# Performance work log

Measured on AMD Instinct MI355X. Metric: run time of the kernel, lower is better.

## Reference

```python
import jax, jax.numpy as jnp
import numpy as np


def setup_inputs() -> dict:
    key = jax.random.key(0)
    ks = jax.random.split(key, 6)
    B, S, D, E = 4, 8192, 2048, 8
    scale = 1.0 / np.sqrt(D)
    return {
        "x": jax.random.normal(ks[0], (B, S, D), dtype=jnp.float32),
        "Wg": jax.random.normal(ks[1], (E, D), dtype=jnp.float32) * scale,
        "bg": jax.random.normal(ks[2], (E,), dtype=jnp.float32) * scale,
        "Wn": jax.random.normal(ks[3], (E, D), dtype=jnp.float32) * scale,
        "bn": jax.random.normal(ks[4], (E,), dtype=jnp.float32) * scale,
        "noise": jax.random.normal(ks[5], (B, S, E), dtype=jnp.float32),
        "k": 2,
    }


def reference(x, Wg, bg, Wn, bn, noise, k):
    # gate and noisy-gate projections: [B,S,D] x [E,D] -> [B,S,E]
    gate_logits = jnp.einsum("bsd,ed->bse", x, Wg) + bg
    noisy_pre = jnp.einsum("bsd,ed->bse", x, Wn) + bn
    noisy_logits = noise * jax.nn.softplus(noisy_pre) + gate_logits

    # top-k over experts (largest, sorted), matching torch.topk
    topklogits, topexperts = jax.lax.top_k(noisy_logits, k)  # [B,S,k]

    # softmax over sparse logits (-inf elsewhere) == softmax over the topk
    # values, scattered back; small E,k so a one-hot scatter is cheap.
    topk_probs = jax.nn.softmax(topklogits, axis=-1)          # [B,S,k]
    onehot = jax.nn.one_hot(topexperts, noisy_logits.shape[-1],
                            dtype=topk_probs.dtype)           # [B,S,k,E]
    router_output = jnp.einsum("bsk,bske->bse", topk_probs, onehot)
    return router_output, topexperts
```

## Files before the change

kernel.cpp:

```cpp
#include <hip/hip_runtime.h>
#include <math.h>


#define RD 2048
#define RE 8
#define NE16 16
#define TOKB 64
#define CH 64
#define KSL 2
#define KLEN (RD / KSL)
#define NCH (KLEN / CH)
#define NW 4
#define REDW 20

#define AS1 __attribute__((address_space(1)))
#define AS3 __attribute__((address_space(3)))

__device__ __forceinline__ void gload_lds16(const float* g, float* l) {
    __builtin_amdgcn_global_load_lds((const AS1 unsigned int*)g,
                                     (AS3 unsigned int*)l, 16, 0, 0);
}

__global__ __launch_bounds__(256) void transpose_w_kernel(
    const float* __restrict__ Wg, const float* __restrict__ Wn,
    float* __restrict__ WT)
{
    const int idx = blockIdx.x * 256 + threadIdx.x;
    const int d = idx >> 4;
    const int e = idx & 15;
    WT[idx] = (e < 8) ? Wg[e * RD + d] : Wn[(e - 8) * RD + d];
}

__global__ __launch_bounds__(256) void router_main_kernel(
    const float* __restrict__ x,
    const float* __restrict__ WT,
    float* __restrict__ pws,
    int T)
{
    __shared__ float xb[2][TOKB * CH];

    const int tid = threadIdx.x;
    const int w = tid >> 6;
    const int l = tid & 63;
    const int kslice = blockIdx.x & 1;
    const int bt = blockIdx.x >> 1;
    const int tokBase = bt * TOKB;
    const int kbase = kslice * KLEN;

    float acc[NE16];
#pragma unroll
    for (int e = 0; e < NE16; ++e) acc[e] = 0.f;

    {
#pragma unroll
        for (int s = 0; s < 4; ++s) {
            const int t = (w * 4 + s) * 4 + (l >> 4);
            const int p = l & 15;
            const float* gsrc = x + (size_t)(tokBase + t) * RD + kbase
                                + ((p ^ (t & 7)) << 2);
            gload_lds16(gsrc, &xb[0][(w * 4 + s) * 256]);
        }
    }
    __syncthreads();

#pragma unroll 1
    for (int c = 0; c < NCH; ++c) {
        const int buf = c & 1;

        if (c + 1 < NCH) {
#pragma unroll
            for (int s = 0; s < 4; ++s) {
                const int t = (w * 4 + s) * 4 + (l >> 4);
                const int p = l & 15;
                const float* gsrc = x + (size_t)(tokBase + t) * RD + kbase
                                    + (c + 1) * CH + ((p ^ (t & 7)) << 2);
                gload_lds16(gsrc, &xb[buf ^ 1][(w * 4 + s) * 256]);
            }
        }

        const int wbase = __builtin_amdgcn_readfirstlane(
            (kbase + c * CH + w * 16) * NE16);
        const float* __restrict__ wt = WT + wbase;
#pragma unroll
        for (int r = 0; r < 4; ++r) {
            const int phys = (w * 4 + r) ^ (l & 7);
            const float4 xq = *reinterpret_cast<const float4*>(
                &xb[buf][l * CH + (phys << 2)]);
            const float xs[4] = {xq.x, xq.y, xq.z, xq.w};
#pragma unroll
            for (int ii = 0; ii < 4; ++ii) {
                const float* wrow = wt + (r * 4 + ii) * NE16;
#pragma unroll
                for (int e = 0; e < NE16; ++e)
                    acc[e] = fmaf(xs[ii], wrow[e], acc[e]);
            }
        }

        __syncthreads();
    }

    float* red = &xb[0][0];
    {
        const int roff = (w * TOKB + l) * REDW;
        *reinterpret_cast<float4*>(&red[roff + 0])  = make_float4(acc[0], acc[1], acc[2], acc[3]);
        *reinterpret_cast<float4*>(&red[roff + 4])  = make_float4(acc[4], acc[5], acc[6], acc[7]);
        *reinterpret_cast<float4*>(&red[roff + 8])  = make_float4(acc[8], acc[9], acc[10], acc[11]);
        *reinterpret_cast<float4*>(&red[roff + 12]) = make_float4(acc[12], acc[13], acc[14], acc[15]);
    }
    __syncthreads();

    {
        const int tok = tid >> 2;
        const int q = tid & 3;
        float4 s = make_float4(0.f, 0.f, 0.f, 0.f);
#pragma unroll
        for (int wv = 0; wv < NW; ++wv) {
            const float4 a = *reinterpret_cast<const float4*>(
                &red[(wv * TOKB + tok) * REDW + q * 4]);
            s.x += a.x; s.y += a.y; s.z += a.z; s.w += a.w;
        }
        float* dst = pws + ((size_t)kslice * T + tokBase + tok) * NE16 + q * 4;
        *reinterpret_cast<float4*>(dst) = s;
    }
}

__global__ __launch_bounds__(256) void router_finalize_kernel(
    const float* __restrict__ pws,
    const float* __restrict__ bg,
    const float* __restrict__ bn,
    const float* __restrict__ noise,
    float* __restrict__ out_router,
    float* __restrict__ out_experts,
    int T)
{
    const int tok = blockIdx.x * 256 + threadIdx.x;

    const float* p0 = pws + (size_t)tok * NE16;
    const float* p1 = pws + ((size_t)T + tok) * NE16;

    float g[RE], nn[RE];
#pragma unroll
    for (int e = 0; e < RE; ++e) {
        g[e]  = p0[e] + p1[e] + bg[e];
        nn[e] = p0[8 + e] + p1[8 + e] + bn[e];
    }

    const float4* nzp = reinterpret_cast<const float4*>(noise + (size_t)tok * RE);
    const float4 nz0 = nzp[0];
    const float4 nz1 = nzp[1];
    const float nzv[RE] = {nz0.x, nz0.y, nz0.z, nz0.w,
                           nz1.x, nz1.y, nz1.z, nz1.w};

    float v[RE];
#pragma unroll
    for (int e = 0; e < RE; ++e) {
        const float p = nn[e];
        const float sp = fmaxf(p, 0.f) + log1pf(expf(-fabsf(p)));
        v[e] = fmaf(nzv[e], sp, g[e]);
    }

    int i1 = 0; float m1 = v[0];
#pragma unroll
    for (int e = 1; e < RE; ++e)
        if (v[e] > m1) { m1 = v[e]; i1 = e; }
    int i2 = -1; float m2 = -INFINITY;
#pragma unroll
    for (int e = 0; e < RE; ++e)
        if (e != i1 && v[e] > m2) { m2 = v[e]; i2 = e; }

    const float e2 = expf(m2 - m1);
    const float inv = 1.f / (1.f + e2);
    const float p1s = inv;
    const float p2s = e2 * inv;

    float r[RE];
#pragma unroll
    for (int e = 0; e < RE; ++e)
        r[e] = (e == i1) ? p1s : ((e == i2) ? p2s : 0.f);

    float4* orow = reinterpret_cast<float4*>(out_router + (size_t)tok * RE);
    orow[0] = make_float4(r[0], r[1], r[2], r[3]);
    orow[1] = make_float4(r[4], r[5], r[6], r[7]);

    float2* erow = reinterpret_cast<float2*>(out_experts + (size_t)tok * 2);
    *erow = make_float2((float)i1, (float)i2);
}

extern "C" void kernel_launch(void* const* d_in, const int* in_sizes, int n_in,
                              void* d_out, int out_size, void* d_ws, size_t ws_size,
                              hipStream_t stream) {
    const float* x   = (const float*)d_in[0];
    const float* Wg  = (const float*)d_in[1];
    const float* bg  = (const float*)d_in[2];
    const float* Wn  = (const float*)d_in[3];
    const float* bn  = (const float*)d_in[4];
    const float* nz  = (const float*)d_in[5];
    const int T = in_sizes[0] / RD;

    float* WT  = (float*)d_ws;
    float* pws = WT + (size_t)RD * NE16;

    float* out_router  = (float*)d_out;
    float* out_experts = out_router + (size_t)T * RE;

    hipLaunchKernelGGL(transpose_w_kernel, dim3((RD * NE16) / 256), dim3(256),
                       0, stream, Wg, Wn, WT);

    const int blocks = (T / TOKB) * KSL;
    hipLaunchKernelGGL(router_main_kernel, dim3(blocks), dim3(256), 0,
                       stream, x, WT, pws, T);

    hipLaunchKernelGGL(router_finalize_kernel, dim3(T / 256), dim3(256), 0,
                       stream, pws, bg, bn, nz, out_router, out_experts, T);
}
```

Measured before the change: 62.23 us.

## Split K into four slices with smaller LDS chunks and kslice-major block order

Templates the main kernel on the number of K slices and launches four slices when the workspace allows, with a two-slice fallback otherwise. The LDS chunk shrinks from 64 to 32 columns, which halves shared memory per block and allows more resident blocks. Blocks are now ordered kslice-major instead of interleaved. The finalize kernel loops over a runtime slice count, so partial-sum traffic to global memory and the reduction work grow in exchange for more parallelism and occupancy.

```diff
diff --git a/kernel.cpp b/kernel.cpp
--- a/kernel.cpp
+++ b/kernel.cpp
@@ -6,12 +6,8 @@
 #define RE 8
 #define NE16 16
 #define TOKB 64
-#define CH 64
-#define KSL 2
-#define KLEN (RD / KSL)
-#define NCH (KLEN / CH)
+#define CH 32
 #define NW 4
-#define REDW 20
 
 #define AS1 __attribute__((address_space(1)))
 #define AS3 __attribute__((address_space(3)))
@@ -31,19 +27,23 @@
     WT[idx] = (e < 8) ? Wg[e * RD + d] : Wn[(e - 8) * RD + d];
 }
 
+template <int KSL>
 __global__ __launch_bounds__(256) void router_main_kernel(
     const float* __restrict__ x,
     const float* __restrict__ WT,
     float* __restrict__ pws,
     int T)
 {
+    constexpr int KLEN = RD / KSL;
+    constexpr int NCH = KLEN / CH;
     __shared__ float xb[2][TOKB * CH];
 
     const int tid = threadIdx.x;
     const int w = tid >> 6;
     const int l = tid & 63;
-    const int kslice = blockIdx.x & 1;
-    const int bt = blockIdx.x >> 1;
+    const int NTB = T / TOKB;
+    const int bt = blockIdx.x % NTB;
+    const int kslice = blockIdx.x / NTB;
     const int tokBase = bt * TOKB;
     const int kbase = kslice * KLEN;
 
@@ -53,12 +53,13 @@
 
     {
 #pragma unroll
-        for (int s = 0; s < 4; ++s) {
-            const int t = (w * 4 + s) * 4 + (l >> 4);
-            const int p = l & 15;
+        for (int s = 0; s < 2; ++s) {
+            const int i = w * 2 + s;
+            const int t = i * 8 + (l >> 3);
+            const int p = l & 7;
             const float* gsrc = x + (size_t)(tokBase + t) * RD + kbase
                                 + ((p ^ (t & 7)) << 2);
-            gload_lds16(gsrc, &xb[0][(w * 4 + s) * 256]);
+            gload_lds16(gsrc, &xb[0][i * 256]);
         }
     }
     __syncthreads();
@@ -69,23 +70,24 @@
 
         if (c + 1 < NCH) {
 #pragma unroll
-            for (int s = 0; s < 4; ++s) {
-                const int t = (w * 4 + s) * 4 + (l >> 4);
-                const int p = l & 15;
+            for (int s = 0; s < 2; ++s) {
+                const int i = w * 2 + s;
+                const int t = i * 8 + (l >> 3);
+                const int p = l & 7;
                 const float* gsrc = x + (size_t)(tokBase + t) * RD + kbase
                                     + (c + 1) * CH + ((p ^ (t & 7)) << 2);
-                gload_lds16(gsrc, &xb[buf ^ 1][(w * 4 + s) * 256]);
+                gload_lds16(gsrc, &xb[buf ^ 1][i * 256]);
             }
         }
 
         const int wbase = __builtin_amdgcn_readfirstlane(
-            (kbase + c * CH + w * 16) * NE16);
+            (kbase + c * CH + w * 8) * NE16);
         const float* __restrict__ wt = WT + wbase;
 #pragma unroll
-        for (int r = 0; r < 4; ++r) {
-            const int phys = (w * 4 + r) ^ (l & 7);
+        for (int r = 0; r < 2; ++r) {
+            const int q = w * 2 + r;
             const float4 xq = *reinterpret_cast<const float4*>(
-                &xb[buf][l * CH + (phys << 2)]);
+                &xb[buf][l * CH + ((q ^ (l & 7)) << 2)]);
             const float xs[4] = {xq.x, xq.y, xq.z, xq.w};
 #pragma unroll
             for (int ii = 0; ii < 4; ++ii) {
@@ -101,7 +103,7 @@
 
     float* red = &xb[0][0];
     {
-        const int roff = (w * TOKB + l) * REDW;
+        const int roff = (w * TOKB + l) * NE16;
         *reinterpret_cast<float4*>(&red[roff + 0])  = make_float4(acc[0], acc[1], acc[2], acc[3]);
         *reinterpret_cast<float4*>(&red[roff + 4])  = make_float4(acc[4], acc[5], acc[6], acc[7]);
         *reinterpret_cast<float4*>(&red[roff + 8])  = make_float4(acc[8], acc[9], acc[10], acc[11]);
@@ -111,15 +113,15 @@
 
     {
         const int tok = tid >> 2;
-        const int q = tid & 3;
+        const int q4 = tid & 3;
         float4 s = make_float4(0.f, 0.f, 0.f, 0.f);
 #pragma unroll
         for (int wv = 0; wv < NW; ++wv) {
             const float4 a = *reinterpret_cast<const float4*>(
-                &red[(wv * TOKB + tok) * REDW + q * 4]);
+                &red[(wv * TOKB + tok) * NE16 + q4 * 4]);
             s.x += a.x; s.y += a.y; s.z += a.z; s.w += a.w;
         }
-        float* dst = pws + ((size_t)kslice * T + tokBase + tok) * NE16 + q * 4;
+        float* dst = pws + ((size_t)kslice * T + tokBase + tok) * NE16 + q4 * 4;
         *reinterpret_cast<float4*>(dst) = s;
     }
 }
@@ -131,18 +133,18 @@
     const float* __restrict__ noise,
     float* __restrict__ out_router,
     float* __restrict__ out_experts,
-    int T)
+    int T, int ksl)
 {
     const int tok = blockIdx.x * 256 + threadIdx.x;
 
-    const float* p0 = pws + (size_t)tok * NE16;
-    const float* p1 = pws + ((size_t)T + tok) * NE16;
-
     float g[RE], nn[RE];
 #pragma unroll
-    for (int e = 0; e < RE; ++e) {
-        g[e]  = p0[e] + p1[e] + bg[e];
-        nn[e] = p0[8 + e] + p1[8 + e] + bn[e];
+    for (int e = 0; e < RE; ++e) { g[e] = bg[e]; nn[e] = bn[e]; }
+#pragma unroll 1
+    for (int s = 0; s < ksl; ++s) {
+        const float* p = pws + ((size_t)s * T + tok) * NE16;
+#pragma unroll
+        for (int e = 0; e < RE; ++e) { g[e] += p[e]; nn[e] += p[8 + e]; }
     }
 
     const float4* nzp = reinterpret_cast<const float4*>(noise + (size_t)tok * RE);
@@ -206,10 +208,19 @@
     hipLaunchKernelGGL(transpose_w_kernel, dim3((RD * NE16) / 256), dim3(256),
                        0, stream, Wg, Wn, WT);
 
-    const int blocks = (T / TOKB) * KSL;
-    hipLaunchKernelGGL(router_main_kernel, dim3(blocks), dim3(256), 0,
-                       stream, x, WT, pws, T);
-
-    hipLaunchKernelGGL(router_finalize_kernel, dim3(T / 256), dim3(256), 0,
-                       stream, pws, bg, bn, nz, out_router, out_experts, T);
-}
+    const int NTB = T / TOKB;
+    const size_t need4 = (size_t)RD * NE16 * 4 + (size_t)4 * T * NE16 * 4;
+    if (ws_size >= need4) {
+        hipLaunchKernelGGL(router_main_kernel<4>, dim3(NTB * 4), dim3(256), 0,
+                           stream, x, WT, pws, T);
+        hipLaunchKernelGGL(router_finalize_kernel, dim3(T / 256), dim3(256), 0,
+                           stream, pws, bg, bn, nz, out_router, out_experts,
+                           T, 4);
+    } else {
+        hipLaunchKernelGGL(router_main_kernel<2>, dim3(NTB * 2), dim3(256), 0,
+                           stream, x, WT, pws, T);
+        hipLaunchKernelGGL(router_finalize_kernel, dim3(T / 256), dim3(256), 0,
+                           stream, pws, bg, bn, nz, out_router, out_experts,
+                           T, 2);
+    }
+}
```

Result: slower. 66.34 us (+6.6%).

## Fuse router finalize into main kernel via last-arriver atomic flag

Applied to the files above, without the earlier changes.

Removes the separate finalize kernel. Each token block's two k-slice partial results are now combined by whichever block finishes last, detected with a per-tile atomic counter and threadfences, and that block then runs the softplus/top-2/softmax epilogue. Block ordering changes so the two k-slices of a tile are half a grid apart, and the LDS reduction stride drops its padding. This saves a kernel launch and a pass over the partials, at the cost of an extra memset launch for the flags, atomics, and possible LDS bank conflicts in the reduction.

```diff
diff --git a/kernel.cpp b/kernel.cpp
--- a/kernel.cpp
+++ b/kernel.cpp
@@ -11,15 +11,6 @@
 #define KLEN (RD / KSL)
 #define NCH (KLEN / CH)
 #define NW 4
-#define REDW 20
-
-#define AS1 __attribute__((address_space(1)))
-#define AS3 __attribute__((address_space(3)))
-
-__device__ __forceinline__ void gload_lds16(const float* g, float* l) {
-    __builtin_amdgcn_global_load_lds((const AS1 unsigned int*)g,
-                                     (AS3 unsigned int*)l, 16, 0, 0);
-}
 
 __global__ __launch_bounds__(256) void transpose_w_kernel(
     const float* __restrict__ Wg, const float* __restrict__ Wn,
@@ -31,10 +22,24 @@
     WT[idx] = (e < 8) ? Wg[e * RD + d] : Wn[(e - 8) * RD + d];
 }
 
+#define AS1 __attribute__((address_space(1)))
+#define AS3 __attribute__((address_space(3)))
+
+__device__ __forceinline__ void gload_lds16(const float* g, float* l) {
+    __builtin_amdgcn_global_load_lds((const AS1 unsigned int*)g,
+                                     (AS3 unsigned int*)l, 16, 0, 0);
+}
+
 __global__ __launch_bounds__(256) void router_main_kernel(
     const float* __restrict__ x,
     const float* __restrict__ WT,
+    const float* __restrict__ bg,
+    const float* __restrict__ bn,
+    const float* __restrict__ noise,
     float* __restrict__ pws,
+    int* __restrict__ flags,
+    float* __restrict__ out_router,
+    float* __restrict__ out_experts,
     int T)
 {
     __shared__ float xb[2][TOKB * CH];
@@ -42,8 +47,9 @@
     const int tid = threadIdx.x;
     const int w = tid >> 6;
     const int l = tid & 63;
-    const int kslice = blockIdx.x & 1;
-    const int bt = blockIdx.x >> 1;
+    const int NTB = T / TOKB;
+    const int bt = blockIdx.x % NTB;
+    const int kslice = blockIdx.x / NTB;
     const int tokBase = bt * TOKB;
     const int kbase = kslice * KLEN;
 
@@ -101,7 +107,7 @@
 
     float* red = &xb[0][0];
     {
-        const int roff = (w * TOKB + l) * REDW;
+        const int roff = (w * TOKB + l) * NE16;
         *reinterpret_cast<float4*>(&red[roff + 0])  = make_float4(acc[0], acc[1], acc[2], acc[3]);
         *reinterpret_cast<float4*>(&red[roff + 4])  = make_float4(acc[4], acc[5], acc[6], acc[7]);
         *reinterpret_cast<float4*>(&red[roff + 8])  = make_float4(acc[8], acc[9], acc[10], acc[11]);
@@ -111,79 +117,78 @@
 
     {
         const int tok = tid >> 2;
-        const int q = tid & 3;
+        const int q4 = tid & 3;
         float4 s = make_float4(0.f, 0.f, 0.f, 0.f);
 #pragma unroll
         for (int wv = 0; wv < NW; ++wv) {
             const float4 a = *reinterpret_cast<const float4*>(
-                &red[(wv * TOKB + tok) * REDW + q * 4]);
+                &red[(wv * TOKB + tok) * NE16 + q4 * 4]);
             s.x += a.x; s.y += a.y; s.z += a.z; s.w += a.w;
         }
-        float* dst = pws + ((size_t)kslice * T + tokBase + tok) * NE16 + q * 4;
+        float* dst = pws + ((size_t)kslice * T + tokBase + tok) * NE16 + q4 * 4;
         *reinterpret_cast<float4*>(dst) = s;
     }
-}
-
-__global__ __launch_bounds__(256) void router_finalize_kernel(
-    const float* __restrict__ pws,
-    const float* __restrict__ bg,
-    const float* __restrict__ bn,
-    const float* __restrict__ noise,
-    float* __restrict__ out_router,
-    float* __restrict__ out_experts,
-    int T)
-{
-    const int tok = blockIdx.x * 256 + threadIdx.x;
-
-    const float* p0 = pws + (size_t)tok * NE16;
-    const float* p1 = pws + ((size_t)T + tok) * NE16;
-
-    float g[RE], nn[RE];
-#pragma unroll
-    for (int e = 0; e < RE; ++e) {
-        g[e]  = p0[e] + p1[e] + bg[e];
-        nn[e] = p0[8 + e] + p1[8 + e] + bn[e];
-    }
-
-    const float4* nzp = reinterpret_cast<const float4*>(noise + (size_t)tok * RE);
-    const float4 nz0 = nzp[0];
-    const float4 nz1 = nzp[1];
-    const float nzv[RE] = {nz0.x, nz0.y, nz0.z, nz0.w,
-                           nz1.x, nz1.y, nz1.z, nz1.w};
-
-    float v[RE];
-#pragma unroll
-    for (int e = 0; e < RE; ++e) {
-        const float p = nn[e];
-        const float sp = fmaxf(p, 0.f) + log1pf(expf(-fabsf(p)));
-        v[e] = fmaf(nzv[e], sp, g[e]);
-    }
-
-    int i1 = 0; float m1 = v[0];
-#pragma unroll
-    for (int e = 1; e < RE; ++e)
-        if (v[e] > m1) { m1 = v[e]; i1 = e; }
-    int i2 = -1; float m2 = -INFINITY;
-#pragma unroll
-    for (int e = 0; e < RE; ++e)
-        if (e != i1 && v[e] > m2) { m2 = v[e]; i2 = e; }
-
-    const float e2 = expf(m2 - m1);
-    const float inv = 1.f / (1.f + e2);
-    const float p1s = inv;
-    const float p2s = e2 * inv;
-
-    float r[RE];
-#pragma unroll
-    for (int e = 0; e < RE; ++e)
-        r[e] = (e == i1) ? p1s : ((e == i2) ? p2s : 0.f);
-
-    float4* orow = reinterpret_cast<float4*>(out_router + (size_t)tok * RE);
-    orow[0] = make_float4(r[0], r[1], r[2], r[3]);
-    orow[1] = make_float4(r[4], r[5], r[6], r[7]);
-
-    float2* erow = reinterpret_cast<float2*>(out_experts + (size_t)tok * 2);
-    *erow = make_float2((float)i1, (float)i2);
+
+    __threadfence();
+    __syncthreads();
+    int* amF = (int*)&red[4096];
+    if (tid == 0) *amF = atomicAdd(flags + bt, 1);
+    __syncthreads();
+    if (*amF != 1) return;
+    __threadfence();
+
+    if (tid < TOKB) {
+        const int tok = tokBase + tid;
+        const float* pp0 = pws + (size_t)tok * NE16;
+        const float* pp1 = pws + ((size_t)T + tok) * NE16;
+
+        float g[RE], nn[RE];
+#pragma unroll
+        for (int e = 0; e < RE; ++e) {
+            g[e]  = pp0[e] + pp1[e] + bg[e];
+            nn[e] = pp0[8 + e] + pp1[8 + e] + bn[e];
+        }
+
+        const float4* nzp = reinterpret_cast<const float4*>(noise + (size_t)tok * RE);
+        const float4 nz0 = nzp[0];
+        const float4 nz1 = nzp[1];
+        const float nzv[RE] = {nz0.x, nz0.y, nz0.z, nz0.w,
+                               nz1.x, nz1.y, nz1.z, nz1.w};
+
+        float v[RE];
+#pragma unroll
+        for (int e = 0; e < RE; ++e) {
+            const float p = nn[e];
+            const float sp = fmaxf(p, 0.f) + log1pf(expf(-fabsf(p)));
+            v[e] = fmaf(nzv[e], sp, g[e]);
+        }
+
+        int i1 = 0; float m1 = v[0];
+#pragma unroll
+        for (int e = 1; e < RE; ++e)
+            if (v[e] > m1) { m1 = v[e]; i1 = e; }
+        int i2 = -1; float m2 = -INFINITY;
+#pragma unroll
+        for (int e = 0; e < RE; ++e)
+            if (e != i1 && v[e] > m2) { m2 = v[e]; i2 = e; }
+
+        const float e2 = expf(m2 - m1);
+        const float inv = 1.f / (1.f + e2);
+        const float p1s = inv;
+        const float p2s = e2 * inv;
+
+        float r[RE];
+#pragma unroll
+        for (int e = 0; e < RE; ++e)
+            r[e] = (e == i1) ? p1s : ((e == i2) ? p2s : 0.f);
+
+        float4* orow = reinterpret_cast<float4*>(out_router + (size_t)tok * RE);
+        orow[0] = make_float4(r[0], r[1], r[2], r[3]);
+        orow[1] = make_float4(r[4], r[5], r[6], r[7]);
+
+        float2* erow = reinterpret_cast<float2*>(out_experts + (size_t)tok * 2);
+        *erow = make_float2((float)i1, (float)i2);
+    }
 }
 
 extern "C" void kernel_launch(void* const* d_in, const int* in_sizes, int n_in,
@@ -196,20 +201,21 @@
     const float* bn  = (const float*)d_in[4];
     const float* nz  = (const float*)d_in[5];
     const int T = in_sizes[0] / RD;
-
-    float* WT  = (float*)d_ws;
-    float* pws = WT + (size_t)RD * NE16;
+    const int NTB = T / TOKB;
+
+    float* WT   = (float*)d_ws;
+    float* pws  = WT + (size_t)RD * NE16;
+    int* flags  = (int*)(pws + (size_t)KSL * T * NE16);
 
     float* out_router  = (float*)d_out;
     float* out_experts = out_router + (size_t)T * RE;
 
+    hipMemsetAsync(flags, 0, NTB * sizeof(int), stream);
+
     hipLaunchKernelGGL(transpose_w_kernel, dim3((RD * NE16) / 256), dim3(256),
                        0, stream, Wg, Wn, WT);
 
-    const int blocks = (T / TOKB) * KSL;
-    hipLaunchKernelGGL(router_main_kernel, dim3(blocks), dim3(256), 0,
-                       stream, x, WT, pws, T);
-
-    hipLaunchKernelGGL(router_finalize_kernel, dim3(T / 256), dim3(256), 0,
-                       stream, pws, bg, bn, nz, out_router, out_experts, T);
-}
+    hipLaunchKernelGGL(router_main_kernel, dim3(NTB * KSL), dim3(256), 0,
+                       stream, x, WT, bg, bn, nz, pws, flags,
+                       out_router, out_experts, T);
+}
```

Result: slower. 183.1 us (+194.3%).
